# Optimization experiments

Hardware: AMD Instinct MI355X
Metric: run time of the kernel (lower is better)

## Reference

```python
import jax, jax.numpy as jnp
import numpy as np

N = 100000
E = 1600000


def gcn_conv(x, W, b, src, dst, n_nodes):
    """PyG GCNConv: linear -> add self loops -> sym-normalized scatter-add."""
    h = x @ W  # [N, out]
    # degree with self-loops: deg[i] = 1 + in_degree(i)
    deg = jax.ops.segment_sum(jnp.ones((src.shape[0],), h.dtype), dst,
                              num_segments=n_nodes) + 1.0
    dinv = jax.lax.rsqrt(deg)  # deg >= 1 always
    norm = dinv[src] * dinv[dst]  # [E]
    # neighbor messages + self-loop contribution (norm = deg^-1)
    agg = jax.ops.segment_sum(h[src] * norm[:, None], dst,
                              num_segments=n_nodes)
    return agg + h * (dinv * dinv)[:, None] + b


def setup_inputs() -> dict:
    key = jax.random.key(0)
    k1, k2, k3, k4 = jax.random.split(key, 4)
    x = jax.random.normal(k1, (N, 128), dtype=jnp.float32)
    edge_index = jax.random.randint(k2, (2, E), 0, N, dtype=jnp.int64)
    W1 = jax.random.normal(k3, (128, 64), dtype=jnp.float32) * (1.0 / np.sqrt(128))
    b1 = jnp.zeros((64,), jnp.float32)
    W2 = jax.random.normal(k4, (64, 40), dtype=jnp.float32) * (1.0 / np.sqrt(64))
    b2 = jnp.zeros((40,), jnp.float32)
    return {"x": x, "edge_index": edge_index, "W1": W1, "b1": b1,
            "W2": W2, "b2": b2}


def reference(x, edge_index, W1, b1, W2, b2):
    src, dst = edge_index[0], edge_index[1]
    h = gcn_conv(x, W1, b1, src, dst, N)
    h = jax.nn.relu(h)
    # dropout is identity in eval mode; mask_features is a no-op
    h = gcn_conv(h, W2, b2, src, dst, N)
    return jax.nn.log_softmax(h, axis=1)
```

## Files before the change

### kernel.cpp

```cpp
#include <hip/hip_runtime.h>
#include <math.h>

#define N_NODES 100000
#define N_EDGES 1600000
#define F_IN    128
#define F_HID   64
#define F_OUT   40

#define BIN_SHIFT 8
#define NBINS     392
#define BIN_CAP   5120
#define FILL_BLOCKS 512

typedef unsigned int  uint;
typedef unsigned short ushort;
typedef __attribute__((ext_vector_type(8))) short bf16x8;
typedef __attribute__((ext_vector_type(4))) float f32x4;

__device__ __forceinline__ unsigned short f2bf(float f) {
    uint u = __float_as_uint(f);
    u = (u + 0x7FFF + ((u >> 16) & 1)) >> 16;
    return (unsigned short)u;
}
__device__ __forceinline__ uint pack2bf(float a, float b) {
    return (uint)f2bf(a) | ((uint)f2bf(b) << 16);
}
__device__ __forceinline__ float bf_lo(uint u) { return __uint_as_float(u << 16); }
__device__ __forceinline__ float bf_hi(uint u) { return __uint_as_float(u & 0xFFFF0000u); }

__global__ void prep_kernel(const float* __restrict__ W, uint* __restrict__ Wt,
                            int* __restrict__ bcursor) {
    int tid = threadIdx.x;
    if (tid < NBINS) bcursor[tid] = tid * BIN_CAP;
    for (int i = tid; i < 4096; i += 512) {
        int c  = i >> 6;
        int kp = i & 63;
        Wt[i] = pack2bf(W[(2 * kp) * F_HID + c], W[(2 * kp + 1) * F_HID + c]);
    }
}

__global__ void binfill_kernel(const int* __restrict__ src, const int* __restrict__ dst,
                               int* __restrict__ bcursor, int* __restrict__ bins, int E) {
    __shared__ int lcount[NBINS];
    __shared__ int gbase[NBINS];
    int tid = threadIdx.x;
    for (int i = tid; i < NBINS; i += 256) lcount[i] = 0;
    __syncthreads();
    int chunk = (E + gridDim.x - 1) / gridDim.x;
    int beg = blockIdx.x * chunk, end = min(E, beg + chunk);
    for (int e = beg + tid; e < end; e += 256)
        atomicAdd(&lcount[dst[e] >> BIN_SHIFT], 1);
    __syncthreads();
    for (int i = tid; i < NBINS; i += 256) {
        gbase[i] = lcount[i] ? atomicAdd(&bcursor[i], lcount[i]) : 0;
        lcount[i] = 0;
    }
    __syncthreads();
    for (int e = beg + tid; e < end; e += 256) {
        int d = dst[e];
        int b = d >> BIN_SHIFT;
        int p = atomicAdd(&lcount[b], 1);
        bins[gbase[b] + p] = src[e] | ((d & 255) << 17);
    }
}

__global__ void binsort_kernel(const int* __restrict__ bcursor, const int* __restrict__ bins,
                               int* __restrict__ csr, int* __restrict__ rowstart,
                               int* __restrict__ rowcnt, float* __restrict__ dinv) {
    __shared__ int hist[256];
    __shared__ int scan[256];
    __shared__ int cur[256];
    __shared__ int sorted[BIN_CAP];
    int b = blockIdx.x, t = threadIdx.x;
    int base = b * BIN_CAP;
    int cnt = bcursor[b] - base;
    if (t < 256) hist[t] = 0;
    __syncthreads();
    for (int i = t; i < cnt; i += 512)
        atomicAdd(&hist[(unsigned)bins[base + i] >> 17], 1);
    __syncthreads();
    int v = 0;
    if (t < 256) { v = hist[t]; scan[t] = v; }
    __syncthreads();
    for (int off = 1; off < 256; off <<= 1) {
        int u = (t < 256 && t >= off) ? scan[t - off] : 0;
        __syncthreads();
        if (t < 256) scan[t] += u;
        __syncthreads();
    }
    if (t < 256) {
        int excl = scan[t] - v;
        cur[t] = excl;
        int node = (b << BIN_SHIFT) + t;
        if (node < N_NODES) {
            rowstart[node] = base + excl;
            rowcnt[node]   = v;
            dinv[node] = rsqrtf((float)v + 1.0f);
        }
    }
    __syncthreads();
    for (int i = t; i < cnt; i += 512) {
        int p   = bins[base + i];
        int pos = atomicAdd(&cur[(unsigned)p >> 17], 1);
        sorted[pos] = p & 0x1FFFF;
    }
    __syncthreads();
    for (int i = t; i < cnt; i += 512)
        csr[base + i] = sorted[i];
}

#define XPITCH 68
__global__ __launch_bounds__(256) void gemm1_kernel(const float* __restrict__ x,
                                                    const uint* __restrict__ Wt,
                                                    ushort* __restrict__ h, int n) {
    __shared__ __align__(16) uint Xu[64 * XPITCH];
    __shared__ __align__(16) uint Wu[64 * XPITCH];
    int tid = threadIdx.x;
    int node0 = blockIdx.x * 64;

    {
        int c = tid >> 2, qq = tid & 3;
        const uint4* gsrc = (const uint4*)&Wt[c * 64 + qq * 16];
        uint4* ldst = (uint4*)&Wu[c * XPITCH + qq * 16];
        #pragma unroll
        for (int j = 0; j < 4; ++j) ldst[j] = gsrc[j];
    }
    {
        int row = tid >> 2, qq = tid & 3;
        int node = node0 + row;
        uint4* ldst = (uint4*)&Xu[row * XPITCH + qq * 16];
        if (node < n) {
            const float4* gsrc = (const float4*)&x[(size_t)node * F_IN + qq * 32];
            #pragma unroll
            for (int j = 0; j < 4; ++j) {
                float4 a = gsrc[2 * j], b = gsrc[2 * j + 1];
                uint4 o;
                o.x = pack2bf(a.x, a.y); o.y = pack2bf(a.z, a.w);
                o.z = pack2bf(b.x, b.y); o.w = pack2bf(b.z, b.w);
                ldst[j] = o;
            }
        } else {
            uint4 z = make_uint4(0, 0, 0, 0);
            #pragma unroll
            for (int j = 0; j < 4; ++j) ldst[j] = z;
        }
    }
    __syncthreads();

    int wv   = tid >> 6;
    int lane = tid & 63;
    int lrow = lane & 15;
    int quad = lane >> 4;

    bf16x8 bfrag[4][4];
    #pragma unroll
    for (int t = 0; t < 4; ++t)
        #pragma unroll
        for (int s = 0; s < 4; ++s)
            bfrag[t][s] = *(const bf16x8*)&Wu[(t * 16 + lrow) * XPITCH + s * 16 + quad * 4];

    f32x4 acc[4];
    #pragma unroll
    for (int t = 0; t < 4; ++t) acc[t] = (f32x4){0.f, 0.f, 0.f, 0.f};

    #pragma unroll
    for (int s = 0; s < 4; ++s) {
        bf16x8 afrag = *(const bf16x8*)&Xu[(wv * 16 + lrow) * XPITCH + s * 16 + quad * 4];
        #pragma unroll
        for (int t = 0; t < 4; ++t)
            acc[t] = __builtin_amdgcn_mfma_f32_16x16x32_bf16(afrag, bfrag[t][s], acc[t], 0, 0, 0);
    }

    #pragma unroll
    for (int t = 0; t < 4; ++t) {
        #pragma unroll
        for (int i = 0; i < 4; ++i) {
            int node = node0 + wv * 16 + quad * 4 + i;
            if (node < n) h[(size_t)node * F_HID + t * 16 + lrow] = f2bf(acc[t][i]);
        }
    }
}

__global__ void agg1_kernel(const int* __restrict__ rowstart, const int* __restrict__ rowcnt,
                            const int* __restrict__ csr, const float* __restrict__ dinv,
                            const ushort* __restrict__ h, const float* __restrict__ b,
                            ushort* __restrict__ out, int n) {
    int node = blockIdx.x * 4 + (threadIdx.x >> 6);
    int lane = threadIdx.x & 63;
    if (node >= n) return;
    int slot = lane >> 3;
    int c    = lane & 7;
    int beg = rowstart[node], end = beg + rowcnt[node];
    float acc[8] = {0.f,0.f,0.f,0.f,0.f,0.f,0.f,0.f};
    for (int base = beg; base < end; base += 64) {
        int idx = base + lane;
        int   sid = 0; float wgt = 0.f;
        if (idx < end) { sid = csr[idx]; wgt = dinv[sid]; }
        int cnt    = min(64, end - base);
        int groups = (cnt + 7) >> 3;
        int g = 0;
        for (; g + 2 <= groups; g += 2) {
            int   sA = __shfl(sid, g * 8 + slot);
            float wA = __shfl(wgt, g * 8 + slot);
            int   sB = __shfl(sid, g * 8 + 8 + slot);
            float wB = __shfl(wgt, g * 8 + 8 + slot);
            uint4 hA = *(const uint4*)&h[(size_t)sA * F_HID + (c << 3)];
            uint4 hB = *(const uint4*)&h[(size_t)sB * F_HID + (c << 3)];
            acc[0] += bf_lo(hA.x) * wA; acc[1] += bf_hi(hA.x) * wA;
            acc[2] += bf_lo(hA.y) * wA; acc[3] += bf_hi(hA.y) * wA;
            acc[4] += bf_lo(hA.z) * wA; acc[5] += bf_hi(hA.z) * wA;
            acc[6] += bf_lo(hA.w) * wA; acc[7] += bf_hi(hA.w) * wA;
            acc[0] += bf_lo(hB.x) * wB; acc[1] += bf_hi(hB.x) * wB;
            acc[2] += bf_lo(hB.y) * wB; acc[3] += bf_hi(hB.y) * wB;
            acc[4] += bf_lo(hB.z) * wB; acc[5] += bf_hi(hB.z) * wB;
            acc[6] += bf_lo(hB.w) * wB; acc[7] += bf_hi(hB.w) * wB;
        }
        if (g < groups) {
            int   sA = __shfl(sid, g * 8 + slot);
            float wA = __shfl(wgt, g * 8 + slot);
            uint4 hA = *(const uint4*)&h[(size_t)sA * F_HID + (c << 3)];
            acc[0] += bf_lo(hA.x) * wA; acc[1] += bf_hi(hA.x) * wA;
            acc[2] += bf_lo(hA.y) * wA; acc[3] += bf_hi(hA.y) * wA;
            acc[4] += bf_lo(hA.z) * wA; acc[5] += bf_hi(hA.z) * wA;
            acc[6] += bf_lo(hA.w) * wA; acc[7] += bf_hi(hA.w) * wA;
        }
    }
    #pragma unroll
    for (int m = 8; m < 64; m <<= 1) {
        #pragma unroll
        for (int k = 0; k < 8; ++k) acc[k] += __shfl_xor(acc[k], m);
    }
    if (slot == 0) {
        float di = dinv[node];
        uint4 hs = *(const uint4*)&h[(size_t)node * F_HID + (c << 3)];
        float self[8] = { bf_lo(hs.x), bf_hi(hs.x), bf_lo(hs.y), bf_hi(hs.y),
                          bf_lo(hs.z), bf_hi(hs.z), bf_lo(hs.w), bf_hi(hs.w) };
        float4 b0 = *(const float4*)&b[c << 3];
        float4 b1v = *(const float4*)&b[(c << 3) + 4];
        float bb[8] = { b0.x, b0.y, b0.z, b0.w, b1v.x, b1v.y, b1v.z, b1v.w };
        ushort o[8];
        #pragma unroll
        for (int k = 0; k < 8; ++k) {
            float v = fmaxf(acc[k] * di + self[k] * di * di + bb[k], 0.f);
            o[k] = f2bf(v);
        }
        uint4 pk;
        pk.x = (uint)o[0] | ((uint)o[1] << 16);
        pk.y = (uint)o[2] | ((uint)o[3] << 16);
        pk.z = (uint)o[4] | ((uint)o[5] << 16);
        pk.w = (uint)o[6] | ((uint)o[7] << 16);
        *(uint4*)&out[(size_t)node * F_HID + (c << 3)] = pk;
    }
}

__global__ void gemm2_kernel(const ushort* __restrict__ a, const float* __restrict__ W,
                             ushort* __restrict__ h, int n) {
    __shared__ float Wl[F_HID * F_OUT];
    int tid = threadIdx.x;
    for (int i = tid; i < F_HID * F_OUT; i += 256) Wl[i] = W[i];
    __syncthreads();
    long long idx = (long long)blockIdx.x * 256 + tid;
    if (idx >= (long long)n * F_OUT) return;
    int node = (int)(idx / F_OUT);
    int col  = (int)(idx - (long long)node * F_OUT);
    const uint* arow = (const uint*)(a + (size_t)node * F_HID);
    float acc = 0.0f;
    #pragma unroll 8
    for (int k = 0; k < F_HID / 2; ++k) {
        uint u = arow[k];
        acc += bf_lo(u) * Wl[(2 * k) * F_OUT + col] + bf_hi(u) * Wl[(2 * k + 1) * F_OUT + col];
    }
    h[idx] = f2bf(acc);
}

__global__ void agg2_kernel(const int* __restrict__ rowstart, const int* __restrict__ rowcnt,
                            const int* __restrict__ csr, const float* __restrict__ dinv,
                            const ushort* __restrict__ h, const float* __restrict__ b,
                            float* __restrict__ out, int n) {
    int node = blockIdx.x * 4 + (threadIdx.x >> 6);
    int lane = threadIdx.x & 63;
    if (node >= n) return;
    int slot = lane / 10;
    int c    = lane - slot * 10;
    int beg = rowstart[node], end = beg + rowcnt[node];
    float acc[4] = {0.f, 0.f, 0.f, 0.f};
    for (int base = beg; base < end; base += 60) {
        int idx = base + lane;
        int   sid = 0; float wgt = 0.f;
        if (lane < 60 && idx < end) { sid = csr[idx]; wgt = dinv[sid]; }
        int cnt    = min(60, end - base);
        int groups = (cnt + 5) / 6;
        int g = 0;
        for (; g + 2 <= groups; g += 2) {
            int   slA = (slot < 6) ? (g * 6 + slot) : 60;
            int   slB = (slot < 6) ? (g * 6 + 6 + slot) : 60;
            int   sA = __shfl(sid, slA);
            float wA = __shfl(wgt, slA);
            int   sB = __shfl(sid, slB);
            float wB = __shfl(wgt, slB);
            uint2 hA = *(const uint2*)&h[(size_t)sA * F_OUT + (c << 2)];
            uint2 hB = *(const uint2*)&h[(size_t)sB * F_OUT + (c << 2)];
            acc[0] += bf_lo(hA.x) * wA; acc[1] += bf_hi(hA.x) * wA;
            acc[2] += bf_lo(hA.y) * wA; acc[3] += bf_hi(hA.y) * wA;
            acc[0] += bf_lo(hB.x) * wB; acc[1] += bf_hi(hB.x) * wB;
            acc[2] += bf_lo(hB.y) * wB; acc[3] += bf_hi(hB.y) * wB;
        }
        if (g < groups) {
            int   slA = (slot < 6) ? (g * 6 + slot) : 60;
            int   sA = __shfl(sid, slA);
            float wA = __shfl(wgt, slA);
            uint2 hA = *(const uint2*)&h[(size_t)sA * F_OUT + (c << 2)];
            acc[0] += bf_lo(hA.x) * wA; acc[1] += bf_hi(hA.x) * wA;
            acc[2] += bf_lo(hA.y) * wA; acc[3] += bf_hi(hA.y) * wA;
        }
    }
    float r[4];
    #pragma unroll
    for (int k = 0; k < 4; ++k) {
        float t3 = __shfl(acc[k], lane + 30);
        float s0 = acc[k] + t3;
        float t1 = __shfl(s0, lane + 10);
        float t2 = __shfl(s0, lane + 20);
        r[k] = s0 + t1 + t2;
    }
    float val[4] = {0.f, 0.f, 0.f, 0.f};
    float m = -INFINITY;
    if (lane < 10) {
        float di = dinv[node];
        uint2 hs = *(const uint2*)&h[(size_t)node * F_OUT + (c << 2)];
        float self[4] = { bf_lo(hs.x), bf_hi(hs.x), bf_lo(hs.y), bf_hi(hs.y) };
        float4 bb = *(const float4*)&b[c << 2];
        float bbv[4] = { bb.x, bb.y, bb.z, bb.w };
        #pragma unroll
        for (int k = 0; k < 4; ++k) {
            val[k] = r[k] * di + self[k] * di * di + bbv[k];
            m = fmaxf(m, val[k]);
        }
    }
    #pragma unroll
    for (int off = 1; off < 16; off <<= 1) m = fmaxf(m, __shfl_xor(m, off));
    float p = 0.f;
    if (lane < 10)
        p = __expf(val[0] - m) + __expf(val[1] - m) + __expf(val[2] - m) + __expf(val[3] - m);
    #pragma unroll
    for (int off = 1; off < 16; off <<= 1) p += __shfl_xor(p, off);
    float lse = m + __logf(p);
    if (lane < 10) {
        float4 o;
        o.x = val[0] - lse; o.y = val[1] - lse; o.z = val[2] - lse; o.w = val[3] - lse;
        *(float4*)&out[(size_t)node * F_OUT + (c << 2)] = o;
    }
}

extern "C" void kernel_launch(void* const* d_in, const int* in_sizes, int n_in,
                              void* d_out, int out_size, void* d_ws, size_t ws_size,
                              hipStream_t stream) {
    const float* x  = (const float*)d_in[0];
    const int*   ei = (const int*)d_in[1];
    const float* W1 = (const float*)d_in[2];
    const float* b1 = (const float*)d_in[3];
    const float* W2 = (const float*)d_in[4];
    const float* b2 = (const float*)d_in[5];
    const int* src = ei;
    const int* dst = ei + N_EDGES;

    char* p = (char*)d_ws;
    int*    bcursor  = (int*)p;     p += (size_t)(NBINS + 8) * 4;
    int*    bins     = (int*)p;     p += (size_t)NBINS * BIN_CAP * 4;
    int*    csr_src  = (int*)p;     p += (size_t)NBINS * BIN_CAP * 4;
    int*    rowstart = (int*)p;     p += (size_t)(N_NODES + 4) * 4;
    int*    rowcnt   = (int*)p;     p += (size_t)(N_NODES + 4) * 4;
    float*  dinv     = (float*)p;   p += (size_t)N_NODES * 4;
    uint*   Wtb      = (uint*)p;    p += (size_t)4096 * 4;
    ushort* h1b      = (ushort*)p;  p += (size_t)N_NODES * F_HID * 2;
    ushort* out1b    = (ushort*)p;  p += (size_t)N_NODES * F_HID * 2;
    ushort* h2b      = (ushort*)p;  p += (size_t)N_NODES * F_OUT * 2;
    float*  out      = (float*)d_out;

    prep_kernel   <<<1, 512, 0, stream>>>(W1, Wtb, bcursor);
    binfill_kernel<<<FILL_BLOCKS, 256, 0, stream>>>(src, dst, bcursor, bins, N_EDGES);
    binsort_kernel<<<NBINS, 512, 0, stream>>>(bcursor, bins, csr_src, rowstart, rowcnt, dinv);
    gemm1_kernel  <<<(N_NODES + 63) / 64, 256, 0, stream>>>(x, Wtb, h1b, N_NODES);
    agg1_kernel   <<<(N_NODES + 3) / 4, 256, 0, stream>>>(rowstart, rowcnt, csr_src, dinv,
                                                          h1b, b1, out1b, N_NODES);
    gemm2_kernel  <<<((N_NODES * F_OUT) + 255) / 256, 256, 0, stream>>>(out1b, W2, h2b, N_NODES);
    agg2_kernel   <<<(N_NODES + 3) / 4, 256, 0, stream>>>(rowstart, rowcnt, csr_src, dinv,
                                                          h2b, b2, out, N_NODES);
}
```

Measured before the change: 285.5 us.

## Fuse second-layer GEMM into layer-1 aggregation epilogue

Result: no change. 290.3 us (+1.7%).

```diff
diff --git a/kernel.cpp b/kernel.cpp
--- a/kernel.cpp
+++ b/kernel.cpp
@@ -181,13 +181,22 @@
     }
 }
 
+#define W2P 41
 __global__ void agg1_kernel(const int* __restrict__ rowstart, const int* __restrict__ rowcnt,
                             const int* __restrict__ csr, const float* __restrict__ dinv,
                             const ushort* __restrict__ h, const float* __restrict__ b,
-                            ushort* __restrict__ out, int n) {
-    int node = blockIdx.x * 4 + (threadIdx.x >> 6);
-    int lane = threadIdx.x & 63;
-    if (node >= n) return;
+                            const float* __restrict__ W2, ushort* __restrict__ h2,
+                            int n) {
+    __shared__ float W2l[F_HID * W2P];
+    int tid = threadIdx.x;
+    for (int i = tid; i < F_HID * F_OUT; i += 256) {
+        int k = i / F_OUT, j = i - k * F_OUT;
+        W2l[k * W2P + j] = W2[i];
+    }
+    __syncthreads();
+
+    int node = blockIdx.x * 4 + (tid >> 6);
+    int lane = tid & 63;
     int slot = lane >> 3;
     int c    = lane & 7;
     int beg = rowstart[node], end = beg + rowcnt[node];
@@ -230,47 +239,32 @@
         #pragma unroll
         for (int k = 0; k < 8; ++k) acc[k] += __shfl_xor(acc[k], m);
     }
-    if (slot == 0) {
-        float di = dinv[node];
-        uint4 hs = *(const uint4*)&h[(size_t)node * F_HID + (c << 3)];
-        float self[8] = { bf_lo(hs.x), bf_hi(hs.x), bf_lo(hs.y), bf_hi(hs.y),
-                          bf_lo(hs.z), bf_hi(hs.z), bf_lo(hs.w), bf_hi(hs.w) };
-        float4 b0 = *(const float4*)&b[c << 3];
-        float4 b1v = *(const float4*)&b[(c << 3) + 4];
-        float bb[8] = { b0.x, b0.y, b0.z, b0.w, b1v.x, b1v.y, b1v.z, b1v.w };
-        ushort o[8];
-        #pragma unroll
-        for (int k = 0; k < 8; ++k) {
-            float v = fmaxf(acc[k] * di + self[k] * di * di + bb[k], 0.f);
-            o[k] = f2bf(v);
-        }
-        uint4 pk;
-        pk.x = (uint)o[0] | ((uint)o[1] << 16);
-        pk.y = (uint)o[2] | ((uint)o[3] << 16);
-        pk.z = (uint)o[4] | ((uint)o[5] << 16);
-        pk.w = (uint)o[6] | ((uint)o[7] << 16);
-        *(uint4*)&out[(size_t)node * F_HID + (c << 3)] = pk;
-    }
-}
-
-__global__ void gemm2_kernel(const ushort* __restrict__ a, const float* __restrict__ W,
-                             ushort* __restrict__ h, int n) {
-    __shared__ float Wl[F_HID * F_OUT];
-    int tid = threadIdx.x;
-    for (int i = tid; i < F_HID * F_OUT; i += 256) Wl[i] = W[i];
-    __syncthreads();
-    long long idx = (long long)blockIdx.x * 256 + tid;
-    if (idx >= (long long)n * F_OUT) return;
-    int node = (int)(idx / F_OUT);
-    int col  = (int)(idx - (long long)node * F_OUT);
-    const uint* arow = (const uint*)(a + (size_t)node * F_HID);
-    float acc = 0.0f;
-    #pragma unroll 8
-    for (int k = 0; k < F_HID / 2; ++k) {
-        uint u = arow[k];
-        acc += bf_lo(u) * Wl[(2 * k) * F_OUT + col] + bf_hi(u) * Wl[(2 * k + 1) * F_OUT + col];
-    }
-    h[idx] = f2bf(acc);
+    float di = dinv[node];
+    uint4 hs = *(const uint4*)&h[(size_t)node * F_HID + (c << 3)];
+    float self[8] = { bf_lo(hs.x), bf_hi(hs.x), bf_lo(hs.y), bf_hi(hs.y),
+                      bf_lo(hs.z), bf_hi(hs.z), bf_lo(hs.w), bf_hi(hs.w) };
+    float4 b0 = *(const float4*)&b[c << 3];
+    float4 b1v = *(const float4*)&b[(c << 3) + 4];
+    float bb[8] = { b0.x, b0.y, b0.z, b0.w, b1v.x, b1v.y, b1v.z, b1v.w };
+    float v[8];
+    #pragma unroll
+    for (int k = 0; k < 8; ++k)
+        v[k] = fmaxf(acc[k] * di + self[k] * di * di + bb[k], 0.f);
+
+    float myh2 = 0.f;
+    #pragma unroll
+    for (int r = 0; r < 5; ++r) {
+        int j = r * 8 + slot;
+        float p = 0.f;
+        #pragma unroll
+        for (int i = 0; i < 8; ++i)
+            p += v[i] * W2l[(c * 8 + i) * W2P + j];
+        p += __shfl_xor(p, 1);
+        p += __shfl_xor(p, 2);
+        p += __shfl_xor(p, 4);
+        if (c == r) myh2 = p;
+    }
+    if (c < 5) h2[(size_t)node * F_OUT + c * 8 + slot] = f2bf(myh2);
 }
 
 __global__ void agg2_kernel(const int* __restrict__ rowstart, const int* __restrict__ rowcnt,
@@ -373,7 +367,6 @@
     float*  dinv     = (float*)p;   p += (size_t)N_NODES * 4;
     uint*   Wtb      = (uint*)p;    p += (size_t)4096 * 4;
     ushort* h1b      = (ushort*)p;  p += (size_t)N_NODES * F_HID * 2;
-    ushort* out1b    = (ushort*)p;  p += (size_t)N_NODES * F_HID * 2;
     ushort* h2b      = (ushort*)p;  p += (size_t)N_NODES * F_OUT * 2;
     float*  out      = (float*)d_out;
 
@@ -381,9 +374,8 @@
     binfill_kernel<<<FILL_BLOCKS, 256, 0, stream>>>(src, dst, bcursor, bins, N_EDGES);
     binsort_kernel<<<NBINS, 512, 0, stream>>>(bcursor, bins, csr_src, rowstart, rowcnt, dinv);
     gemm1_kernel  <<<(N_NODES + 63) / 64, 256, 0, stream>>>(x, Wtb, h1b, N_NODES);
-    agg1_kernel   <<<(N_NODES + 3) / 4, 256, 0, stream>>>(rowstart, rowcnt, csr_src, dinv,
-                                                          h1b, b1, out1b, N_NODES);
-    gemm2_kernel  <<<((N_NODES * F_OUT) + 255) / 256, 256, 0, stream>>>(out1b, W2, h2b, N_NODES);
+    agg1_kernel   <<<N_NODES / 4, 256, 0, stream>>>(rowstart, rowcnt, csr_src, dinv,
+                                                    h1b, b1, W2, h2b, N_NODES);
     agg2_kernel   <<<(N_NODES + 3) / 4, 256, 0, stream>>>(rowstart, rowcnt, csr_src, dinv,
                                                           h2b, b2, out, N_NODES);
 }
```

## Merge edge binning and first GEMM into one launch to overlap them

Applied to the files above, without the earlier changes.

Result: no change. 282.0 us (-1.2%).

```diff
diff --git a/kernel.cpp b/kernel.cpp
--- a/kernel.cpp
+++ b/kernel.cpp
@@ -11,6 +11,7 @@
 #define NBINS     392
 #define BIN_CAP   5120
 #define FILL_BLOCKS 512
+#define GEMM1_BLOCKS ((N_NODES + 63) / 64)
 
 typedef unsigned int  uint;
 typedef unsigned short ushort;
@@ -39,84 +40,42 @@
     }
 }
 
-__global__ void binfill_kernel(const int* __restrict__ src, const int* __restrict__ dst,
-                               int* __restrict__ bcursor, int* __restrict__ bins, int E) {
-    __shared__ int lcount[NBINS];
-    __shared__ int gbase[NBINS];
+#define XPITCH 68
+__global__ __launch_bounds__(256) void fillgemm_kernel(
+        const int* __restrict__ src, const int* __restrict__ dst,
+        int* __restrict__ bcursor, int* __restrict__ bins, int E,
+        const float* __restrict__ x, const uint* __restrict__ Wt,
+        ushort* __restrict__ h, int n) {
+    __shared__ __align__(16) uint smem[2 * 64 * XPITCH];
     int tid = threadIdx.x;
-    for (int i = tid; i < NBINS; i += 256) lcount[i] = 0;
-    __syncthreads();
-    int chunk = (E + gridDim.x - 1) / gridDim.x;
-    int beg = blockIdx.x * chunk, end = min(E, beg + chunk);
-    for (int e = beg + tid; e < end; e += 256)
-        atomicAdd(&lcount[dst[e] >> BIN_SHIFT], 1);
-    __syncthreads();
-    for (int i = tid; i < NBINS; i += 256) {
-        gbase[i] = lcount[i] ? atomicAdd(&bcursor[i], lcount[i]) : 0;
-        lcount[i] = 0;
-    }
-    __syncthreads();
-    for (int e = beg + tid; e < end; e += 256) {
-        int d = dst[e];
-        int b = d >> BIN_SHIFT;
-        int p = atomicAdd(&lcount[b], 1);
-        bins[gbase[b] + p] = src[e] | ((d & 255) << 17);
-    }
-}
-
-__global__ void binsort_kernel(const int* __restrict__ bcursor, const int* __restrict__ bins,
-                               int* __restrict__ csr, int* __restrict__ rowstart,
-                               int* __restrict__ rowcnt, float* __restrict__ dinv) {
-    __shared__ int hist[256];
-    __shared__ int scan[256];
-    __shared__ int cur[256];
-    __shared__ int sorted[BIN_CAP];
-    int b = blockIdx.x, t = threadIdx.x;
-    int base = b * BIN_CAP;
-    int cnt = bcursor[b] - base;
-    if (t < 256) hist[t] = 0;
-    __syncthreads();
-    for (int i = t; i < cnt; i += 512)
-        atomicAdd(&hist[(unsigned)bins[base + i] >> 17], 1);
-    __syncthreads();
-    int v = 0;
-    if (t < 256) { v = hist[t]; scan[t] = v; }
-    __syncthreads();
-    for (int off = 1; off < 256; off <<= 1) {
-        int u = (t < 256 && t >= off) ? scan[t - off] : 0;
-        __syncthreads();
-        if (t < 256) scan[t] += u;
-        __syncthreads();
-    }
-    if (t < 256) {
-        int excl = scan[t] - v;
-        cur[t] = excl;
-        int node = (b << BIN_SHIFT) + t;
-        if (node < N_NODES) {
-            rowstart[node] = base + excl;
-            rowcnt[node]   = v;
-            dinv[node] = rsqrtf((float)v + 1.0f);
-        }
-    }
-    __syncthreads();
-    for (int i = t; i < cnt; i += 512) {
-        int p   = bins[base + i];
-        int pos = atomicAdd(&cur[(unsigned)p >> 17], 1);
-        sorted[pos] = p & 0x1FFFF;
-    }
-    __syncthreads();
-    for (int i = t; i < cnt; i += 512)
-        csr[base + i] = sorted[i];
-}
-
-#define XPITCH 68
-__global__ __launch_bounds__(256) void gemm1_kernel(const float* __restrict__ x,
-                                                    const uint* __restrict__ Wt,
-                                                    ushort* __restrict__ h, int n) {
-    __shared__ __align__(16) uint Xu[64 * XPITCH];
-    __shared__ __align__(16) uint Wu[64 * XPITCH];
-    int tid = threadIdx.x;
-    int node0 = blockIdx.x * 64;
+
+    if (blockIdx.x < FILL_BLOCKS) {
+        int* lcount = (int*)smem;
+        int* gbase  = ((int*)smem) + NBINS;
+        for (int i = tid; i < NBINS; i += 256) lcount[i] = 0;
+        __syncthreads();
+        int chunk = (E + FILL_BLOCKS - 1) / FILL_BLOCKS;
+        int beg = blockIdx.x * chunk, end = min(E, beg + chunk);
+        for (int e = beg + tid; e < end; e += 256)
+            atomicAdd(&lcount[dst[e] >> BIN_SHIFT], 1);
+        __syncthreads();
+        for (int i = tid; i < NBINS; i += 256) {
+            gbase[i] = lcount[i] ? atomicAdd(&bcursor[i], lcount[i]) : 0;
+            lcount[i] = 0;
+        }
+        __syncthreads();
+        for (int e = beg + tid; e < end; e += 256) {
+            int d = dst[e];
+            int b = d >> BIN_SHIFT;
+            int p = atomicAdd(&lcount[b], 1);
+            bins[gbase[b] + p] = src[e] | ((d & 255) << 17);
+        }
+        return;
+    }
+
+    uint* Xu = smem;
+    uint* Wu = smem + 64 * XPITCH;
+    int node0 = (blockIdx.x - FILL_BLOCKS) * 64;
 
     {
         int c = tid >> 2, qq = tid & 3;
@@ -179,6 +138,51 @@
             if (node < n) h[(size_t)node * F_HID + t * 16 + lrow] = f2bf(acc[t][i]);
         }
     }
+}
+
+__global__ void binsort_kernel(const int* __restrict__ bcursor, const int* __restrict__ bins,
+                               int* __restrict__ csr, int* __restrict__ rowstart,
+                               int* __restrict__ rowcnt, float* __restrict__ dinv) {
+    __shared__ int hist[256];
+    __shared__ int scan[256];
+    __shared__ int cur[256];
+    __shared__ int sorted[BIN_CAP];
+    int b = blockIdx.x, t = threadIdx.x;
+    int base = b * BIN_CAP;
+    int cnt = bcursor[b] - base;
+    if (t < 256) hist[t] = 0;
+    __syncthreads();
+    for (int i = t; i < cnt; i += 512)
+        atomicAdd(&hist[(unsigned)bins[base + i] >> 17], 1);
+    __syncthreads();
+    int v = 0;
+    if (t < 256) { v = hist[t]; scan[t] = v; }
+    __syncthreads();
+    for (int off = 1; off < 256; off <<= 1) {
+        int u = (t < 256 && t >= off) ? scan[t - off] : 0;
+        __syncthreads();
+        if (t < 256) scan[t] += u;
+        __syncthreads();
+    }
+    if (t < 256) {
+        int excl = scan[t] - v;
+        cur[t] = excl;
+        int node = (b << BIN_SHIFT) + t;
+        if (node < N_NODES) {
+            rowstart[node] = base + excl;
+            rowcnt[node]   = v;
+            dinv[node] = rsqrtf((float)v + 1.0f);
+        }
+    }
+    __syncthreads();
+    for (int i = t; i < cnt; i += 512) {
+        int p   = bins[base + i];
+        int pos = atomicAdd(&cur[(unsigned)p >> 17], 1);
+        sorted[pos] = p & 0x1FFFF;
+    }
+    __syncthreads();
+    for (int i = t; i < cnt; i += 512)
+        csr[base + i] = sorted[i];
 }
 
 __global__ void agg1_kernel(const int* __restrict__ rowstart, const int* __restrict__ rowcnt,
@@ -377,13 +381,13 @@
     ushort* h2b      = (ushort*)p;  p += (size_t)N_NODES * F_OUT * 2;
     float*  out      = (float*)d_out;
 
-    prep_kernel   <<<1, 512, 0, stream>>>(W1, Wtb, bcursor);
-    binfill_kernel<<<FILL_BLOCKS, 256, 0, stream>>>(src, dst, bcursor, bins, N_EDGES);
-    binsort_kernel<<<NBINS, 512, 0, stream>>>(bcursor, bins, csr_src, rowstart, rowcnt, dinv);
-    gemm1_kernel  <<<(N_NODES + 63) / 64, 256, 0, stream>>>(x, Wtb, h1b, N_NODES);
-    agg1_kernel   <<<(N_NODES + 3) / 4, 256, 0, stream>>>(rowstart, rowcnt, csr_src, dinv,
-                                                          h1b, b1, out1b, N_NODES);
-    gemm2_kernel  <<<((N_NODES * F_OUT) + 255) / 256, 256, 0, stream>>>(out1b, W2, h2b, N_NODES);
-    agg2_kernel   <<<(N_NODES + 3) / 4, 256, 0, stream>>>(rowstart, rowcnt, csr_src, dinv,
-                                                          h2b, b2, out, N_NODES);
-}
+    prep_kernel    <<<1, 512, 0, stream>>>(W1, Wtb, bcursor);
+    fillgemm_kernel<<<FILL_BLOCKS + GEMM1_BLOCKS, 256, 0, stream>>>(
+        src, dst, bcursor, bins, N_EDGES, x, Wtb, h1b, N_NODES);
+    binsort_kernel <<<NBINS, 512, 0, stream>>>(bcursor, bins, csr_src, rowstart, rowcnt, dinv);
+    agg1_kernel    <<<(N_NODES + 3) / 4, 256, 0, stream>>>(rowstart, rowcnt, csr_src, dinv,
+                                                           h1b, b1, out1b, N_NODES);
+    gemm2_kernel   <<<((N_NODES * F_OUT) + 255) / 256, 256, 0, stream>>>(out1b, W2, h2b, N_NODES);
+    agg2_kernel    <<<(N_NODES + 3) / 4, 256, 0, stream>>>(rowstart, rowcnt, csr_src, dinv,
+                                                           h2b, b2, out, N_NODES);
+}
```
